# Kernel optimization log

Hardware: AMD Instinct MI355X
Metric: run time of the kernel (lower is better)

The kernel has to match this reference:

```python
import jax, jax.numpy as jnp
import numpy as np

# --- constants from init_kwargs / globals in source ---
HIDDEN = 512
SAMPLE_RATE = 22050
HOP_LENGTH = 256
MAX_DURATION = 10
MIN_DURATION = 1
TARGET_FRAMES = SAMPLE_RATE * MAX_DURATION // HOP_LENGTH  # 861
B, T = 64, 512


def setup_inputs() -> dict:
    key = jax.random.key(0)
    k1, k2 = jax.random.split(key)
    batch = jax.random.normal(k1, (B, T, HIDDEN), dtype=jnp.float32)
    predicted_durations = jax.random.uniform(
        k2, (B, T, 1), dtype=jnp.float32, minval=0.0, maxval=float(MAX_DURATION))
    return {"batch": batch, "predicted_durations": predicted_durations}


def reference(batch, predicted_durations):
    # [B, T] integer per-token frame counts
    d = jnp.round(jnp.clip(predicted_durations, MIN_DURATION, MAX_DURATION))
    d = d.astype(jnp.int32)[..., 0]
    ends = jnp.cumsum(d, axis=1)          # [B, T] exclusive end offset of each token
    total = ends[:, -1]                   # [B] total expanded frames per example
    frames = jnp.arange(TARGET_FRAMES, dtype=jnp.int32)  # [L]
    # For output frame j, source token = first token whose cumulative end > j.
    idx = jax.vmap(lambda e: jnp.searchsorted(e, frames, side='right'))(ends)  # [B, L]
    idx_c = jnp.minimum(idx, batch.shape[1] - 1)
    out = jnp.take_along_axis(batch, idx_c[..., None], axis=1)  # [B, L, H]
    # Frames past the total expanded length are zero-padding; truncation to
    # TARGET_FRAMES is implicit since we only materialize L frames.
    valid = (frames[None, :] < total[:, None]).astype(batch.dtype)  # [B, L]
    return out * valid[..., None]
```

## Files before the change

### kernel.cpp

```cpp
#include <hip/hip_runtime.h>

#define NB 64
#define NT 512
#define HIDDEN 512
#define TARGET_FRAMES 861
#define INVALID_IDX 0xFFFFu
#define NFRAMES (NB * TARGET_FRAMES)
#define GATHER_BLOCKS (NFRAMES / 4)

__global__ __launch_bounds__(NT) void lr_prep(const float* __restrict__ pred,
                                              unsigned short* __restrict__ idxbuf) {
    __shared__ int s[NT];
    __shared__ int wsum[NT / 64];
    const int b = blockIdx.x;
    const int t = threadIdx.x;
    const int lane = t & 63;
    const int wid = t >> 6;

    float p = fminf(fmaxf(pred[b * NT + t], 1.0f), 10.0f);
    int x = (int)rintf(p);
    #pragma unroll
    for (int off = 1; off < 64; off <<= 1) {
        int y = __shfl_up(x, off, 64);
        if (lane >= off) x += y;
    }
    if (lane == 63) wsum[wid] = x;
    __syncthreads();
    int prefix = 0;
    #pragma unroll
    for (int w = 0; w < NT / 64; ++w)
        if (w < wid) prefix += wsum[w];
    x += prefix;
    s[t] = x;
    __syncthreads();

    const int total = s[NT - 1];
    for (int f = t; f < TARGET_FRAMES; f += NT) {
        unsigned short r = INVALID_IDX;
        if (f < total) {
            int lo = 0, hi = NT;
            while (lo < hi) {
                int mid = (lo + hi) >> 1;
                if (s[mid] <= f) lo = mid + 1; else hi = mid;
            }
            r = (unsigned short)min(lo, NT - 1);
        }
        idxbuf[b * TARGET_FRAMES + f] = r;
    }
}

__global__ __launch_bounds__(256) void lr_gather(const float4* __restrict__ batch4,
                                                 const unsigned short* __restrict__ idxbuf,
                                                 float4* __restrict__ out4) {
    const int bid = blockIdx.x;
    const int swz = (bid & 7) * (GATHER_BLOCKS >> 3) + (bid >> 3);
    const int wave = threadIdx.x >> 6;
    const int lane = threadIdx.x & 63;
    const int fi = swz * 4 + wave;
    const int b = fi / TARGET_FRAMES;

    const unsigned int idx = idxbuf[fi];
    float4 v0 = make_float4(0.f, 0.f, 0.f, 0.f);
    float4 v1 = v0;
    if (idx != INVALID_IDX) {
        const float4* src = batch4 + (((size_t)b * NT + idx) << 7);
        v0 = src[lane];
        v1 = src[lane + 64];
    }
    float4* dst = out4 + ((size_t)fi << 7);
    dst[lane] = v0;
    dst[lane + 64] = v1;
}

extern "C" void kernel_launch(void* const* d_in, const int* in_sizes, int n_in,
                              void* d_out, int out_size, void* d_ws, size_t ws_size,
                              hipStream_t stream) {
    const float* batch = (const float*)d_in[0];
    const float* pred  = (const float*)d_in[1];
    float* out = (float*)d_out;
    unsigned short* idxbuf = (unsigned short*)d_ws;

    lr_prep<<<NB, NT, 0, stream>>>(pred, idxbuf);
    lr_gather<<<GATHER_BLOCKS, 256, 0, stream>>>((const float4*)batch, idxbuf,
                                                 (float4*)out);
}
```

Before: 30.15 us.

## Fuse duration prefix-sum and gather into one kernel with per-chunk index computation

Merges the prep kernel and the gather kernel into one launch. Each of 2048 blocks recomputes the batch row's duration prefix sum (two tokens per thread), binary-searches indices for its 27 frames into shared memory, then copies those frame rows. This drops a kernel launch, the workspace index round trip, and the dependency between kernels. The cost is a redundant 512-token scan in every block and fewer frames per block to hide latency.

```diff
diff --git a/kernel.cpp b/kernel.cpp
--- a/kernel.cpp
+++ b/kernel.cpp
@@ -3,22 +3,32 @@
 #define NB 64
 #define NT 512
 #define HIDDEN 512
-#define TARGET_FRAMES 861
-#define INVALID_IDX 0xFFFFu
-#define NFRAMES (NB * TARGET_FRAMES)
-#define GATHER_BLOCKS (NFRAMES / 4)
+#define TF 861
+#define CHUNKS 32
+#define FPC 27
+#define GRID (NB * CHUNKS)
 
-__global__ __launch_bounds__(NT) void lr_prep(const float* __restrict__ pred,
-                                              unsigned short* __restrict__ idxbuf) {
+__global__ __launch_bounds__(256) void lr_fused(const float* __restrict__ pred,
+                                                const float4* __restrict__ batch4,
+                                                float4* __restrict__ out4) {
     __shared__ int s[NT];
-    __shared__ int wsum[NT / 64];
-    const int b = blockIdx.x;
+    __shared__ int wsum[4];
+    __shared__ int sidx[FPC];
+
+    const int bid = blockIdx.x;
+    const int sid = (bid & 7) * (GRID >> 3) + (bid >> 3);
+    const int b = sid >> 5;
+    const int chunk = sid & 31;
+    const int base = chunk * FPC;
+
     const int t = threadIdx.x;
     const int lane = t & 63;
     const int wid = t >> 6;
 
-    float p = fminf(fmaxf(pred[b * NT + t], 1.0f), 10.0f);
-    int x = (int)rintf(p);
+    float2 p2 = ((const float2*)(pred + b * NT))[t];
+    int d0 = (int)rintf(fminf(fmaxf(p2.x, 1.f), 10.f));
+    int d1 = (int)rintf(fminf(fmaxf(p2.y, 1.f), 10.f));
+    int x = d0 + d1;
     #pragma unroll
     for (int off = 1; off < 64; off <<= 1) {
         int y = __shfl_up(x, off, 64);
@@ -28,48 +38,42 @@
     __syncthreads();
     int prefix = 0;
     #pragma unroll
-    for (int w = 0; w < NT / 64; ++w)
+    for (int w = 0; w < 3; ++w)
         if (w < wid) prefix += wsum[w];
     x += prefix;
-    s[t] = x;
+    s[2 * t]     = x - d1;
+    s[2 * t + 1] = x;
     __syncthreads();
 
     const int total = s[NT - 1];
-    for (int f = t; f < TARGET_FRAMES; f += NT) {
-        unsigned short r = INVALID_IDX;
-        if (f < total) {
+
+    if (t < FPC) {
+        int f = base + t;
+        int r = -1;
+        if (f < TF && f < total) {
             int lo = 0, hi = NT;
             while (lo < hi) {
                 int mid = (lo + hi) >> 1;
                 if (s[mid] <= f) lo = mid + 1; else hi = mid;
             }
-            r = (unsigned short)min(lo, NT - 1);
+            r = min(lo, NT - 1);
         }
-        idxbuf[b * TARGET_FRAMES + f] = r;
+        sidx[t] = r;
     }
-}
+    __syncthreads();
 
-__global__ __launch_bounds__(256) void lr_gather(const float4* __restrict__ batch4,
-                                                 const unsigned short* __restrict__ idxbuf,
-                                                 float4* __restrict__ out4) {
-    const int bid = blockIdx.x;
-    const int swz = (bid & 7) * (GATHER_BLOCKS >> 3) + (bid >> 3);
-    const int wave = threadIdx.x >> 6;
-    const int lane = threadIdx.x & 63;
-    const int fi = swz * 4 + wave;
-    const int b = fi / TARGET_FRAMES;
-
-    const unsigned int idx = idxbuf[fi];
-    float4 v0 = make_float4(0.f, 0.f, 0.f, 0.f);
-    float4 v1 = v0;
-    if (idx != INVALID_IDX) {
-        const float4* src = batch4 + (((size_t)b * NT + idx) << 7);
-        v0 = src[lane];
-        v1 = src[lane + 64];
+    const int c = t & 127;
+    const int half = t >> 7;
+    const float4* srcb = batch4 + ((size_t)b << 16);
+    #pragma unroll 2
+    for (int fo = half; fo < FPC; fo += 2) {
+        const int f = base + fo;
+        if (f >= TF) continue;
+        const int idx = sidx[fo];
+        float4 v = make_float4(0.f, 0.f, 0.f, 0.f);
+        if (idx >= 0) v = srcb[(idx << 7) + c];
+        out4[(((size_t)b * TF + f) << 7) + c] = v;
     }
-    float4* dst = out4 + ((size_t)fi << 7);
-    dst[lane] = v0;
-    dst[lane + 64] = v1;
 }
 
 extern "C" void kernel_launch(void* const* d_in, const int* in_sizes, int n_in,
@@ -78,9 +82,6 @@
     const float* batch = (const float*)d_in[0];
     const float* pred  = (const float*)d_in[1];
     float* out = (float*)d_out;
-    unsigned short* idxbuf = (unsigned short*)d_ws;
 
-    lr_prep<<<NB, NT, 0, stream>>>(pred, idxbuf);
-    lr_gather<<<GATHER_BLOCKS, 256, 0, stream>>>((const float4*)batch, idxbuf,
-                                                 (float4*)out);
+    lr_fused<<<GRID, 256, 0, stream>>>(pred, (const float4*)batch, (float4*)out);
 }
```

Result: faster. 27.65 us (-8.3%).
